# Optimization experiments

Measured on AMD Instinct MI355X. Metric: run time of the kernel, lower is better.

## Reference

```python
import jax, jax.numpy as jnp
import numpy as np

L, B, H, R = 128, 4, 768, 24
LN_EPS = 1e-5


def setup_inputs() -> dict:
    key = jax.random.key(0)
    ks = jax.random.split(key, 10)
    s = 1.0 / np.sqrt(H)
    return {
        "h_re": jax.random.normal(ks[0], (L, B, H), jnp.float32),
        "h_share": jax.random.normal(ks[1], (L, B, H), jnp.float32),
        "mask": jnp.ones((L, B), jnp.float32),
        # r: Linear(2H -> H)
        "r_w": jax.random.normal(ks[2], (H, 2 * H), jnp.float32) * s,
        "r_b": jnp.zeros((H,), jnp.float32),
        # hid2hid: Linear(3H -> H)
        "hid_w": jax.random.normal(ks[3], (H, 3 * H), jnp.float32) * s,
        "hid_b": jnp.zeros((H,), jnp.float32),
        # LayerNorm(H)
        "ln_g": jnp.ones((H,), jnp.float32),
        "ln_b": jnp.zeros((H,), jnp.float32),
        # hid2rel: Linear(H -> R)
        "rel_w": jax.random.normal(ks[4], (R, H), jnp.float32) * s,
        "rel_b": jnp.zeros((R,), jnp.float32),
    }


def reference(h_re, h_share, mask, r_w, r_b, hid_w, hid_b, ln_g, ln_b, rel_w, rel_b):
    # h_global = max_over_length( tanh( Linear([h_share; h_re]) ) )  -> [B, H]
    # Decompose concat-linear into two additive projections (same math).
    w_sh, w_re = r_w[:, :H], r_w[:, H:]
    g = jnp.tanh(jnp.einsum('lbh,kh->lbk', h_share, w_sh)
                 + jnp.einsum('lbh,kh->lbk', h_re, w_re) + r_b)
    g = jnp.max(g, axis=0)  # [B, H]

    # hid2hid(cat(r1, r2, g)) = h_re@W1^T (bcast over j) + h_re@W2^T (bcast over i) + g@W3^T + b
    w1, w2, w3 = hid_w[:, :H], hid_w[:, H:2 * H], hid_w[:, 2 * H:]
    p1 = jnp.einsum('lbh,kh->lbk', h_re, w1)        # [L, B, H] -> varies with i
    p2 = jnp.einsum('lbh,kh->lbk', h_re, w2)        # [L, B, H] -> varies with j
    pg = jnp.einsum('bh,kh->bk', g, w3) + hid_b     # [B, H]
    z = p1[:, None, :, :] + p2[None, :, :, :] + pg  # [L, L, B, H]

    # LayerNorm over last dim
    mu = jnp.mean(z, axis=-1, keepdims=True)
    var = jnp.mean(jnp.square(z - mu), axis=-1, keepdims=True)
    z = (z - mu) * jax.lax.rsqrt(var + LN_EPS) * ln_g + ln_b

    # ELU (dropout = identity in eval), then sigmoid(hid2rel)
    z = jax.nn.elu(z)
    re = jax.nn.sigmoid(jnp.einsum('ijbh,rh->ijbr', z, rel_w) + rel_b)  # [L, L, B, R]

    # pairwise mask: mask[i,b] * mask[j,b]
    m = mask[:, None, :] * mask[None, :, :]        # [L, L, B]
    return re * m[..., None]
```

## Files before the change

kernel.cpp:

```cpp
#include <hip/hip_runtime.h>
#include <hip/hip_bf16.h>
#include <math.h>

#define L 128
#define B 4
#define H 768
#define LN_EPS 1e-5f
#define XROWS 272

typedef __attribute__((ext_vector_type(8))) short short8;
typedef __attribute__((ext_vector_type(4))) float f32x4;

static __device__ __forceinline__ unsigned f2bfu(float f) {
    unsigned u = __float_as_uint(f);
    return (u + 0x7FFFu + ((u >> 16) & 1u)) >> 16;
}
static __device__ __forceinline__ uint2 pk4(float4 v) {
    uint2 o;
    o.x = f2bfu(v.x) | (f2bfu(v.y) << 16);
    o.y = f2bfu(v.z) | (f2bfu(v.w) << 16);
    return o;
}
static __device__ __forceinline__ unsigned short f2b(float f) {
    union { __hip_bfloat16 h; unsigned short u; } cv;
    cv.h = __float2bfloat16(f);
    return cv.u;
}
static __device__ __forceinline__ unsigned fkey(float x) {
    unsigned u = __float_as_uint(x);
    return (u >> 31) ? ~u : (u | 0x80000000u);
}

__global__ __launch_bounds__(256) void kConv(const float* __restrict__ h_re,
                                             const float* __restrict__ h_share,
                                             const float* __restrict__ r_w,
                                             const float* __restrict__ hid_w,
                                             const float* __restrict__ rel_w,
                                             unsigned short* __restrict__ apack,
                                             unsigned short* __restrict__ wpackA,
                                             unsigned short* __restrict__ wpackB,
                                             unsigned short* __restrict__ rwb16,
                                             unsigned int* __restrict__ gmax) {
    int t = blockIdx.x * 256 + threadIdx.x;
    if (t >= 397056) return;
    if (t < 98304) {
        int m = t / 192, oct = t % 192, k = oct * 8;
        const float* src = (k < 768) ? (h_share + (size_t)m * 768 + k)
                                     : (h_re + (size_t)m * 768 + k - 768);
        float4 x = *(const float4*)src, y = *(const float4*)(src + 4);
        int mt = m >> 4, lr = m & 15, ks = k >> 5, lq = (k >> 3) & 3;
        uint2* dst = (uint2*)(apack + (((size_t)mt * 48 + ks) * 64 + lq * 16 + lr) * 8);
        dst[0] = pk4(x); dst[1] = pk4(y);
    } else if (t < 245760) {
        int t2 = t - 98304;
        int n = t2 / 192, oct = t2 % 192, k = oct * 8;
        const float* src = r_w + (size_t)n * 1536 + k;
        float4 x = *(const float4*)src, y = *(const float4*)(src + 4);
        int nt = n >> 4, lr = n & 15, ks = k >> 5, lq = (k >> 3) & 3;
        uint2* dst = (uint2*)(wpackA + (((size_t)nt * 48 + ks) * 64 + lq * 16 + lr) * 8);
        dst[0] = pk4(x); dst[1] = pk4(y);
    } else if (t < 393216) {
        int t3 = t - 245760;
        int n = t3 / 96, oct = t3 % 96, k = oct * 8;
        int half = (n >= 768) ? 1 : 0;
        const float* src = hid_w + (size_t)(n - half * 768) * 2304 + half * 768 + k;
        float4 x = *(const float4*)src, y = *(const float4*)(src + 4);
        int nt = n >> 4, lr = n & 15, ks = k >> 5, lq = (k >> 3) & 3;
        uint2* dst = (uint2*)(wpackB + (((size_t)nt * 24 + ks) * 64 + lq * 16 + lr) * 8);
        dst[0] = pk4(x); dst[1] = pk4(y);
    } else if (t < 396288) {
        int t4 = t - 393216;
        int nt = t4 / 1536, ks = (t4 / 64) % 24, l = t4 & 63;
        int row = nt * 16 + (l & 15);
        int k = ks * 32 + (l >> 4) * 8;
        uint2 o0 = make_uint2(0u, 0u), o1 = o0;
        if (row < 24) {
            const float* src = rel_w + (size_t)row * 768 + k;
            o0 = pk4(*(const float4*)src);
            o1 = pk4(*(const float4*)(src + 4));
        }
        uint2* dst = (uint2*)(rwb16 + (size_t)t4 * 8);
        dst[0] = o0; dst[1] = o1;
    } else {
        int t6 = t - 396288;
        gmax[t6] = 0u;
        gmax[768 + t6] = 0u;
        gmax[1536 + t6] = 0u;
        gmax[2304 + t6] = 0u;
    }
}

template<int KSW>
static __device__ __forceinline__ void gemm_steps(const unsigned short* __restrict__ a0p,
                                                  const unsigned short* __restrict__ a1p,
                                                  const unsigned short* __restrict__ w0p,
                                                  const unsigned short* __restrict__ w1p,
                                                  f32x4 acc[2][2]) {
#pragma unroll
    for (int s = 0; s < KSW; s++) {
        short8 a0 = *(const short8*)(a0p + (size_t)s * 512);
        short8 a1 = *(const short8*)(a1p + (size_t)s * 512);
        short8 w0 = *(const short8*)(w0p + (size_t)s * 512);
        short8 w1 = *(const short8*)(w1p + (size_t)s * 512);
        acc[0][0] = __builtin_amdgcn_mfma_f32_16x16x32_bf16(a0, w0, acc[0][0], 0, 0, 0);
        acc[0][1] = __builtin_amdgcn_mfma_f32_16x16x32_bf16(a0, w1, acc[0][1], 0, 0, 0);
        acc[1][0] = __builtin_amdgcn_mfma_f32_16x16x32_bf16(a1, w0, acc[1][0], 0, 0, 0);
        acc[1][1] = __builtin_amdgcn_mfma_f32_16x16x32_bf16(a1, w1, acc[1][1], 0, 0, 0);
    }
}

__global__ __launch_bounds__(256) void kGemm(const unsigned short* __restrict__ apack,
                                             const unsigned short* __restrict__ wpackA,
                                             const unsigned short* __restrict__ wpackB,
                                             unsigned int* __restrict__ gmax,
                                             unsigned short* __restrict__ xb16,
                                             unsigned short* __restrict__ vpack) {
    __shared__ float red[4][4][64][4];
    int id = blockIdx.x;
    int tid = threadIdx.x, lane = tid & 63, wv = tid >> 6;
    int lq = lane >> 4, lr = lane & 15;
    bool isA = id < 384;
    f32x4 acc[2][2] = {{{0.f,0.f,0.f,0.f},{0.f,0.f,0.f,0.f}},
                       {{0.f,0.f,0.f,0.f},{0.f,0.f,0.f,0.f}}};
    int mt0, nt0;
    if (isA) {
        mt0 = (id / 24) * 2; nt0 = (id % 24) * 2;
        const unsigned short* a0p = apack + ((size_t)mt0 * 48 + wv * 12) * 512 + lane * 8;
        const unsigned short* w0p = wpackA + ((size_t)nt0 * 48 + wv * 12) * 512 + lane * 8;
        gemm_steps<12>(a0p, a0p + 48 * 512, w0p, w0p + 48 * 512, acc);
    } else {
        int id2 = id - 384;
        mt0 = (id2 / 48) * 2; nt0 = (id2 % 48) * 2;
        const unsigned short* a0p = apack + ((size_t)mt0 * 48 + 24 + wv * 6) * 512 + lane * 8;
        const unsigned short* w0p = wpackB + ((size_t)nt0 * 24 + wv * 6) * 512 + lane * 8;
        gemm_steps<6>(a0p, a0p + 48 * 512, w0p, w0p + 24 * 512, acc);
    }
#pragma unroll
    for (int mi = 0; mi < 2; mi++)
#pragma unroll
        for (int ni = 0; ni < 2; ni++)
            *(f32x4*)&red[wv][mi * 2 + ni][lane][0] = acc[mi][ni];
    __syncthreads();
    if (wv != 0) return;

    f32x4 s2[2][2];
#pragma unroll
    for (int mi = 0; mi < 2; mi++)
#pragma unroll
        for (int ni = 0; ni < 2; ni++) {
            f32x4 v = *(f32x4*)&red[0][mi * 2 + ni][lane][0];
#pragma unroll
            for (int w = 1; w < 4; w++) {
                f32x4 u = *(f32x4*)&red[w][mi * 2 + ni][lane][0];
                v[0] += u[0]; v[1] += u[1]; v[2] += u[2]; v[3] += u[3];
            }
            s2[mi][ni] = v;
        }

    if (isA) {
#pragma unroll
        for (int ni = 0; ni < 2; ni++)
#pragma unroll
            for (int q = 0; q < 4; q++) {
                float mx = fmaxf(s2[0][ni][q], s2[1][ni][q]);
                mx = fmaxf(mx, __shfl_xor(mx, 16, 64));
                mx = fmaxf(mx, __shfl_xor(mx, 32, 64));
                if (lq == 0) {
                    int n = (nt0 + ni) * 16 + lr;
                    atomicMax(&gmax[q * 768 + n], fkey(mx));
                }
            }
    } else {
#pragma unroll
        for (int mi = 0; mi < 2; mi++)
#pragma unroll
            for (int ni = 0; ni < 2; ni++)
#pragma unroll
                for (int q = 0; q < 4; q++) {
                    int m = (mt0 + mi) * 16 + lq * 4 + q;
                    int n = (nt0 + ni) * 16 + lr;
                    int b = m & 3, l = m >> 2;
                    unsigned short val = f2b(s2[mi][ni][q]);
                    if (n < 768) {
                        xb16[((size_t)b * XROWS + l) * 768 + n] = val;
                    } else {
                        int k = n - 768;
                        size_t dst = ((((size_t)(b * 8 + (l >> 4)) * 24) + (k >> 5)) * 64
                                      + ((k >> 3) & 3) * 16 + (l & 15)) * 8 + (k & 7);
                        vpack[dst] = val;
                    }
                }
    }
}

__global__ __launch_bounds__(256) void kPg(const unsigned int* __restrict__ gmax,
                                           const float* __restrict__ r_b,
                                           const float* __restrict__ hid_w,
                                           const float* __restrict__ hid_b,
                                           unsigned short* __restrict__ xb16) {
    __shared__ float sg[768];
    __shared__ float sp[4][64];
    int kt = blockIdx.x, b = blockIdx.y, tid = threadIdx.x;
    for (int v = tid; v < 768; v += 256) {
        unsigned key = gmax[b * 768 + v];
        unsigned bits = (key & 0x80000000u) ? (key & 0x7FFFFFFFu) : ~key;
        sg[v] = tanhf(__uint_as_float(bits) + r_b[v]);
    }
    __syncthreads();
    int kk = tid & 63, hc = tid >> 6;
    int k = kt * 64 + kk;
    const float4* w4 = (const float4*)hid_w;
    const float4* g4 = (const float4*)sg;
    float acc = 0.f;
    for (int h = hc * 48; h < hc * 48 + 48; h++) {
        float4 gv = g4[h];
        float4 wv = w4[(size_t)k * 576 + 384 + h];
        acc += gv.x * wv.x + gv.y * wv.y + gv.z * wv.z + gv.w * wv.w;
    }
    sp[hc][kk] = acc;
    __syncthreads();
    if (hc == 0) {
        float pgv = sp[0][kk] + sp[1][kk] + sp[2][kk] + sp[3][kk] + hid_b[k];
        xb16[((size_t)b * XROWS + 256) * 768 + k] = f2b(pgv);
    }
}

__global__ __launch_bounds__(64, 4) void kC(const unsigned short* __restrict__ xb16,
                                            const unsigned short* __restrict__ vpack,
                                            const float* __restrict__ ln_g,
                                            const float* __restrict__ ln_b,
                                            const unsigned short* __restrict__ rwb16,
                                            const float* __restrict__ rel_b,
                                            const float* __restrict__ mask,
                                            float* __restrict__ out) {
    int i = blockIdx.x, b = blockIdx.y, jg = blockIdx.z;
    int lane = threadIdx.x;
    int lr = lane & 15, lh = lane >> 4;

    const unsigned short* p1r = xb16 + ((size_t)b * XROWS + i) * 768;
    const unsigned short* pgr = xb16 + ((size_t)b * XROWS + 256) * 768;
    const unsigned short* vfr = vpack + (((size_t)(b * 8 + jg) * 24) * 64 + (size_t)lane) * 8;

    float s1 = 0.f, s2 = 0.f;
#pragma unroll 4
    for (int s = 0; s < 24; s++) {
        int k = s * 32 + lh * 8;
        uint4 vv = *(const uint4*)(vfr + (size_t)s * 512);
        uint4 uu = *(const uint4*)(p1r + k);
        uint4 pp = *(const uint4*)(pgr + k);
        const unsigned* vw = (const unsigned*)&vv;
        const unsigned* uw = (const unsigned*)&uu;
        const unsigned* pw = (const unsigned*)&pp;
#pragma unroll
        for (int h = 0; h < 4; h++) {
            float z0 = __uint_as_float(vw[h] << 16) + __uint_as_float(uw[h] << 16)
                     + __uint_as_float(pw[h] << 16);
            float z1 = __uint_as_float(vw[h] & 0xffff0000u) + __uint_as_float(uw[h] & 0xffff0000u)
                     + __uint_as_float(pw[h] & 0xffff0000u);
            s1 += z0 + z1;
            s2 = fmaf(z0, z0, fmaf(z1, z1, s2));
        }
    }
    s1 += __shfl_xor(s1, 16, 64); s1 += __shfl_xor(s1, 32, 64);
    s2 += __shfl_xor(s2, 16, 64); s2 += __shfl_xor(s2, 32, 64);
    float mu  = s1 * (1.f / 768.f);
    float rs  = rsqrtf(s2 * (1.f / 768.f) - mu * mu + LN_EPS);
    float nmr = -mu * rs;

    f32x4 acc0 = {0.f, 0.f, 0.f, 0.f}, acc1 = {0.f, 0.f, 0.f, 0.f};
#pragma unroll 2
    for (int s = 0; s < 24; s++) {
        int k = s * 32 + lh * 8;
        uint4 vv = *(const uint4*)(vfr + (size_t)s * 512);
        uint4 uu = *(const uint4*)(p1r + k);
        uint4 pp = *(const uint4*)(pgr + k);
        float4 g0 = *(const float4*)(ln_g + k), g1 = *(const float4*)(ln_g + k + 4);
        float4 b0 = *(const float4*)(ln_b + k), b1 = *(const float4*)(ln_b + k + 4);
        const unsigned* vw = (const unsigned*)&vv;
        const unsigned* uw = (const unsigned*)&uu;
        const unsigned* pw = (const unsigned*)&pp;
        float ge[8] = {g0.x, g0.y, g0.z, g0.w, g1.x, g1.y, g1.z, g1.w};
        float be[8] = {b0.x, b0.y, b0.z, b0.w, b1.x, b1.y, b1.z, b1.w};
        short8 a;
#pragma unroll
        for (int h = 0; h < 4; h++) {
            float z0 = __uint_as_float(vw[h] << 16) + __uint_as_float(uw[h] << 16)
                     + __uint_as_float(pw[h] << 16);
            float z1 = __uint_as_float(vw[h] & 0xffff0000u) + __uint_as_float(uw[h] & 0xffff0000u)
                     + __uint_as_float(pw[h] & 0xffff0000u);
            float t0 = fmaf(fmaf(z0, rs, nmr), ge[2 * h], be[2 * h]);
            float t1 = fmaf(fmaf(z1, rs, nmr), ge[2 * h + 1], be[2 * h + 1]);
            t0 = fmaxf(t0, __expf(fminf(t0, 0.f)) - 1.f);
            t1 = fmaxf(t1, __expf(fminf(t1, 0.f)) - 1.f);
            a[2 * h]     = (short)f2b(t0);
            a[2 * h + 1] = (short)f2b(t1);
        }
        short8 bf0 = *(const short8*)(rwb16 + ((size_t)s * 64 + lane) * 8);
        short8 bf1 = *(const short8*)(rwb16 + ((size_t)(24 + s) * 64 + lane) * 8);
        acc0 = __builtin_amdgcn_mfma_f32_16x16x32_bf16(a, bf0, acc0, 0, 0, 0);
        acc1 = __builtin_amdgcn_mfma_f32_16x16x32_bf16(a, bf1, acc1, 0, 0, 0);
    }

    float mi_ = mask[i * 4 + b];
#pragma unroll
    for (int q = 0; q < 4; q++) {
        int jglob = jg * 16 + lh * 4 + q;
        float mval = mi_ * mask[jglob * 4 + b];
        size_t ob = ((size_t)(i * 128 + jglob) * 4 + b) * 24;
        out[ob + lr] = mval / (1.f + __expf(-(acc0[q] + rel_b[lr])));
        if (lr < 8)
            out[ob + 16 + lr] = mval / (1.f + __expf(-(acc1[q] + rel_b[16 + lr])));
    }
}

extern "C" void kernel_launch(void* const* d_in, const int* in_sizes, int n_in,
                              void* d_out, int out_size, void* d_ws, size_t ws_size,
                              hipStream_t stream) {
    const float* h_re    = (const float*)d_in[0];
    const float* h_share = (const float*)d_in[1];
    const float* mask    = (const float*)d_in[2];
    const float* r_w     = (const float*)d_in[3];
    const float* r_b     = (const float*)d_in[4];
    const float* hid_w   = (const float*)d_in[5];
    const float* hid_b   = (const float*)d_in[6];
    const float* ln_g    = (const float*)d_in[7];
    const float* ln_b    = (const float*)d_in[8];
    const float* rel_w   = (const float*)d_in[9];
    const float* rel_b   = (const float*)d_in[10];
    float* out = (float*)d_out;

    float* ws = (float*)d_ws;
    unsigned short* apack  = (unsigned short*)(ws);
    unsigned short* wpackA = (unsigned short*)(ws + 393216);
    unsigned short* wpackB = (unsigned short*)(ws + 983040);
    unsigned short* xb16   = (unsigned short*)(ws + 1572864);
    unsigned short* vpack  = (unsigned short*)(ws + 1990656);
    unsigned int*   gmax   = (unsigned int*)(ws + 2187264);
    unsigned short* rwb16  = (unsigned short*)(ws + 2190336);

    kConv<<<1552, 256, 0, stream>>>(h_re, h_share, r_w, hid_w, rel_w,
                                    apack, wpackA, wpackB, rwb16, gmax);
    kGemm<<<1152, 256, 0, stream>>>(apack, wpackA, wpackB, gmax, xb16, vpack);
    kPg<<<dim3(12, 4), 256, 0, stream>>>(gmax, r_b, hid_w, hid_b, xb16);
    kC<<<dim3(128, 4, 8), 64, 0, stream>>>(xb16, vpack, ln_g, ln_b, rwb16,
                                           rel_b, mask, out);
}
```

Before: 70.53 us.

## Compute LayerNorm statistics algebraically from row sums and cross dot products

Removes the per-pair statistics pass in kC by expanding the mean and variance of z = p1_i + p2_j + pg. That expansion needs per-row sums and squared sums, the cross dot-product matrix p1·p2^T (an MFMA GEMM in a new kDotS kernel), and dot products with pg, which a new single-kernel-per-batch kPgX produces. kGemm also writes p1 in the packed MFMA layout so these GEMMs can read it. In exchange there is an extra launch, and the pg matvec now runs on only 4 blocks, which may serialize the hid_w reads. Computing variance as E[z²]-mu² also raises the risk of cancellation error.

```diff
diff --git a/kernel.cpp b/kernel.cpp
--- a/kernel.cpp
+++ b/kernel.cpp
@@ -25,6 +25,9 @@
     union { __hip_bfloat16 h; unsigned short u; } cv;
     cv.h = __float2bfloat16(f);
     return cv.u;
+}
+static __device__ __forceinline__ float b2f(unsigned short u) {
+    return __uint_as_float(((unsigned)u) << 16);
 }
 static __device__ __forceinline__ unsigned fkey(float x) {
     unsigned u = __float_as_uint(x);
@@ -114,7 +117,8 @@
                                              const unsigned short* __restrict__ wpackB,
                                              unsigned int* __restrict__ gmax,
                                              unsigned short* __restrict__ xb16,
-                                             unsigned short* __restrict__ vpack) {
+                                             unsigned short* __restrict__ vpack,
+                                             unsigned short* __restrict__ p1pack) {
     __shared__ float red[4][4][64][4];
     int id = blockIdx.x;
     int tid = threadIdx.x, lane = tid & 63, wv = tid >> 6;
@@ -183,6 +187,9 @@
                     unsigned short val = f2b(s2[mi][ni][q]);
                     if (n < 768) {
                         xb16[((size_t)b * XROWS + l) * 768 + n] = val;
+                        size_t dst = ((((size_t)(b * 8 + (l >> 4)) * 24) + (n >> 5)) * 64
+                                      + ((n >> 3) & 3) * 16 + (l & 15)) * 8 + (n & 7);
+                        p1pack[dst] = val;
                     } else {
                         int k = n - 768;
                         size_t dst = ((((size_t)(b * 8 + (l >> 4)) * 24) + (k >> 5)) * 64
@@ -193,35 +200,154 @@
     }
 }
 
-__global__ __launch_bounds__(256) void kPg(const unsigned int* __restrict__ gmax,
-                                           const float* __restrict__ r_b,
-                                           const float* __restrict__ hid_w,
-                                           const float* __restrict__ hid_b,
-                                           unsigned short* __restrict__ xb16) {
+__global__ __launch_bounds__(256) void kDotS(const unsigned short* __restrict__ p1pack,
+                                             const unsigned short* __restrict__ vpack,
+                                             float* __restrict__ Dp,
+                                             float* __restrict__ Sp1,
+                                             float* __restrict__ Sp1q,
+                                             float* __restrict__ Sv1,
+                                             float* __restrict__ Sv2) {
+    __shared__ float red[4][4][64][4];
+    int id = blockIdx.x;
+    int tid = threadIdx.x, lane = tid & 63, wv = tid >> 6;
+    int lq = lane >> 4, lr = lane & 15;
+    if (id < 64) {
+        int b = id >> 4, tile = id & 15, it = tile >> 2, jt = tile & 3;
+        f32x4 acc[2][2] = {{{0.f,0.f,0.f,0.f},{0.f,0.f,0.f,0.f}},
+                           {{0.f,0.f,0.f,0.f},{0.f,0.f,0.f,0.f}}};
+        const unsigned short* a0p = p1pack + (((size_t)(b * 8 + it * 2) * 24) + wv * 6) * 512 + lane * 8;
+        const unsigned short* a1p = p1pack + (((size_t)(b * 8 + it * 2 + 1) * 24) + wv * 6) * 512 + lane * 8;
+        const unsigned short* w0p = vpack + (((size_t)(b * 8 + jt * 2) * 24) + wv * 6) * 512 + lane * 8;
+        const unsigned short* w1p = vpack + (((size_t)(b * 8 + jt * 2 + 1) * 24) + wv * 6) * 512 + lane * 8;
+        gemm_steps<6>(a0p, a1p, w0p, w1p, acc);
+#pragma unroll
+        for (int mi = 0; mi < 2; mi++)
+#pragma unroll
+            for (int ni = 0; ni < 2; ni++)
+                *(f32x4*)&red[wv][mi * 2 + ni][lane][0] = acc[mi][ni];
+        __syncthreads();
+        if (wv != 0) return;
+#pragma unroll
+        for (int mi = 0; mi < 2; mi++)
+#pragma unroll
+            for (int ni = 0; ni < 2; ni++) {
+                f32x4 v = *(f32x4*)&red[0][mi * 2 + ni][lane][0];
+#pragma unroll
+                for (int w = 1; w < 4; w++) {
+                    f32x4 u = *(f32x4*)&red[w][mi * 2 + ni][lane][0];
+                    v[0] += u[0]; v[1] += u[1]; v[2] += u[2]; v[3] += u[3];
+                }
+#pragma unroll
+                for (int q = 0; q < 4; q++) {
+                    int i = it * 32 + mi * 16 + lq * 4 + q;
+                    int j = jt * 32 + ni * 16 + lr;
+                    Dp[((size_t)b * 128 + i) * 128 + j] = v[q];
+                }
+            }
+    } else {
+        int t = (id - 64) * 4 + wv;
+        bool isP = t < 32;
+        int t2 = t & 31;
+        int b = t2 >> 3, tile = t2 & 7;
+        const unsigned short* src = (isP ? p1pack : vpack)
+                                    + ((size_t)(b * 8 + tile) * 24) * 512 + lane * 8;
+        float s1 = 0.f, sq = 0.f;
+        for (int s = 0; s < 24; s++) {
+            uint4 x = *(const uint4*)(src + (size_t)s * 512);
+            const unsigned* xw = (const unsigned*)&x;
+#pragma unroll
+            for (int h = 0; h < 4; h++) {
+                float e0 = __uint_as_float(xw[h] << 16);
+                float e1 = __uint_as_float(xw[h] & 0xffff0000u);
+                s1 += e0 + e1;
+                sq = fmaf(e0, e0, fmaf(e1, e1, sq));
+            }
+        }
+        s1 += __shfl_xor(s1, 16, 64); s1 += __shfl_xor(s1, 32, 64);
+        sq += __shfl_xor(sq, 16, 64); sq += __shfl_xor(sq, 32, 64);
+        if (lq == 0) {
+            int row = tile * 16 + lr;
+            if (isP) { Sp1[b * 128 + row] = s1; Sp1q[b * 128 + row] = sq; }
+            else     { Sv1[b * 128 + row] = s1; Sv2[b * 128 + row] = sq; }
+        }
+    }
+}
+
+__global__ __launch_bounds__(256) void kPgX(const unsigned int* __restrict__ gmax,
+                                            const float* __restrict__ r_b,
+                                            const float* __restrict__ hid_w,
+                                            const float* __restrict__ hid_b,
+                                            const unsigned short* __restrict__ p1pack,
+                                            const unsigned short* __restrict__ vpack,
+                                            unsigned short* __restrict__ xb16,
+                                            float* __restrict__ Spg,
+                                            float* __restrict__ Spg2,
+                                            float* __restrict__ Cp1,
+                                            float* __restrict__ Cv) {
     __shared__ float sg[768];
-    __shared__ float sp[4][64];
-    int kt = blockIdx.x, b = blockIdx.y, tid = threadIdx.x;
+    __shared__ float spg[768];
+    __shared__ float rbuf[8];
+    int b = blockIdx.x, tid = threadIdx.x;
+    int lane = tid & 63, wv = tid >> 6, lq = lane >> 4, lr = lane & 15;
+
     for (int v = tid; v < 768; v += 256) {
         unsigned key = gmax[b * 768 + v];
         unsigned bits = (key & 0x80000000u) ? (key & 0x7FFFFFFFu) : ~key;
         sg[v] = tanhf(__uint_as_float(bits) + r_b[v]);
     }
     __syncthreads();
-    int kk = tid & 63, hc = tid >> 6;
-    int k = kt * 64 + kk;
     const float4* w4 = (const float4*)hid_w;
     const float4* g4 = (const float4*)sg;
-    float acc = 0.f;
-    for (int h = hc * 48; h < hc * 48 + 48; h++) {
-        float4 gv = g4[h];
-        float4 wv = w4[(size_t)k * 576 + 384 + h];
-        acc += gv.x * wv.x + gv.y * wv.y + gv.z * wv.z + gv.w * wv.w;
-    }
-    sp[hc][kk] = acc;
+#pragma unroll
+    for (int kk = 0; kk < 3; kk++) {
+        int k = tid + kk * 256;
+        float acc = 0.f;
+        for (int h = 0; h < 192; h++) {
+            float4 gv = g4[h];
+            float4 ww = w4[(size_t)k * 576 + 384 + h];
+            acc += gv.x * ww.x + gv.y * ww.y + gv.z * ww.z + gv.w * ww.w;
+        }
+        unsigned short pb = f2b(acc + hid_b[k]);
+        xb16[((size_t)b * XROWS + 256) * 768 + k] = pb;
+        spg[k] = b2f(pb);
+    }
     __syncthreads();
-    if (hc == 0) {
-        float pgv = sp[0][kk] + sp[1][kk] + sp[2][kk] + sp[3][kk] + hid_b[k];
-        xb16[((size_t)b * XROWS + 256) * 768 + k] = f2b(pgv);
+    float l1 = 0.f, l2 = 0.f;
+    for (int v = tid; v < 768; v += 256) { float x = spg[v]; l1 += x; l2 = fmaf(x, x, l2); }
+#pragma unroll
+    for (int off = 32; off > 0; off >>= 1) {
+        l1 += __shfl_xor(l1, off, 64);
+        l2 += __shfl_xor(l2, off, 64);
+    }
+    if (lane == 0) { rbuf[wv] = l1; rbuf[4 + wv] = l2; }
+    __syncthreads();
+    if (tid == 0) {
+        Spg[b]  = rbuf[0] + rbuf[1] + rbuf[2] + rbuf[3];
+        Spg2[b] = rbuf[4] + rbuf[5] + rbuf[6] + rbuf[7];
+    }
+    for (int gi = 0; gi < 4; gi++) {
+        int g = wv + gi * 4;
+        int side = g >> 3, tile = g & 7;
+        const unsigned short* src = (side ? vpack : p1pack)
+                                    + ((size_t)(b * 8 + tile) * 24) * 512 + lane * 8;
+        float d = 0.f;
+        for (int s = 0; s < 24; s++) {
+            uint4 x = *(const uint4*)(src + (size_t)s * 512);
+            const unsigned* xw = (const unsigned*)&x;
+            int kb = s * 32 + lq * 8;
+#pragma unroll
+            for (int h = 0; h < 4; h++) {
+                float e0 = __uint_as_float(xw[h] << 16);
+                float e1 = __uint_as_float(xw[h] & 0xffff0000u);
+                d = fmaf(e0, spg[kb + 2 * h], fmaf(e1, spg[kb + 2 * h + 1], d));
+            }
+        }
+        d += __shfl_xor(d, 16, 64); d += __shfl_xor(d, 32, 64);
+        if (lq == 0) {
+            int row = tile * 16 + lr;
+            if (side) Cv[b * 128 + row] = d;
+            else      Cp1[b * 128 + row] = d;
+        }
     }
 }
 
@@ -232,40 +358,32 @@
                                             const unsigned short* __restrict__ rwb16,
                                             const float* __restrict__ rel_b,
                                             const float* __restrict__ mask,
+                                            const float* __restrict__ Dp,
+                                            const float* __restrict__ Sp1,
+                                            const float* __restrict__ Sp1q,
+                                            const float* __restrict__ Sv1,
+                                            const float* __restrict__ Sv2,
+                                            const float* __restrict__ Spg,
+                                            const float* __restrict__ Spg2,
+                                            const float* __restrict__ Cp1,
+                                            const float* __restrict__ Cv,
                                             float* __restrict__ out) {
     int i = blockIdx.x, b = blockIdx.y, jg = blockIdx.z;
     int lane = threadIdx.x;
     int lr = lane & 15, lh = lane >> 4;
+    int j = jg * 16 + lr;
+
+    float s1 = Sp1[b * 128 + i] + Spg[b] + Sv1[b * 128 + j];
+    float s2 = Sp1q[b * 128 + i] + Spg2[b] + Sv2[b * 128 + j]
+             + 2.f * (Dp[((size_t)b * 128 + i) * 128 + j]
+                      + Cp1[b * 128 + i] + Cv[b * 128 + j]);
+    float mu  = s1 * (1.f / 768.f);
+    float rs  = rsqrtf(s2 * (1.f / 768.f) - mu * mu + LN_EPS);
+    float nmr = -mu * rs;
 
     const unsigned short* p1r = xb16 + ((size_t)b * XROWS + i) * 768;
     const unsigned short* pgr = xb16 + ((size_t)b * XROWS + 256) * 768;
     const unsigned short* vfr = vpack + (((size_t)(b * 8 + jg) * 24) * 64 + (size_t)lane) * 8;
-
-    float s1 = 0.f, s2 = 0.f;
-#pragma unroll 4
-    for (int s = 0; s < 24; s++) {
-        int k = s * 32 + lh * 8;
-        uint4 vv = *(const uint4*)(vfr + (size_t)s * 512);
-        uint4 uu = *(const uint4*)(p1r + k);
-        uint4 pp = *(const uint4*)(pgr + k);
-        const unsigned* vw = (const unsigned*)&vv;
-        const unsigned* uw = (const unsigned*)&uu;
-        const unsigned* pw = (const unsigned*)&pp;
-#pragma unroll
-        for (int h = 0; h < 4; h++) {
-            float z0 = __uint_as_float(vw[h] << 16) + __uint_as_float(uw[h] << 16)
-                     + __uint_as_float(pw[h] << 16);
-            float z1 = __uint_as_float(vw[h] & 0xffff0000u) + __uint_as_float(uw[h] & 0xffff0000u)
-                     + __uint_as_float(pw[h] & 0xffff0000u);
-            s1 += z0 + z1;
-            s2 = fmaf(z0, z0, fmaf(z1, z1, s2));
-        }
-    }
-    s1 += __shfl_xor(s1, 16, 64); s1 += __shfl_xor(s1, 32, 64);
-    s2 += __shfl_xor(s2, 16, 64); s2 += __shfl_xor(s2, 32, 64);
-    float mu  = s1 * (1.f / 768.f);
-    float rs  = rsqrtf(s2 * (1.f / 768.f) - mu * mu + LN_EPS);
-    float nmr = -mu * rs;
 
     f32x4 acc0 = {0.f, 0.f, 0.f, 0.f}, acc1 = {0.f, 0.f, 0.f, 0.f};
 #pragma unroll 2
@@ -335,13 +453,27 @@
     unsigned short* wpackB = (unsigned short*)(ws + 983040);
     unsigned short* xb16   = (unsigned short*)(ws + 1572864);
     unsigned short* vpack  = (unsigned short*)(ws + 1990656);
-    unsigned int*   gmax   = (unsigned int*)(ws + 2187264);
-    unsigned short* rwb16  = (unsigned short*)(ws + 2190336);
+    unsigned short* p1pack = (unsigned short*)(ws + 2187264);
+    float*          Dp     = ws + 2383872;
+    unsigned int*   gmax   = (unsigned int*)(ws + 2449408);
+    unsigned short* rwb16  = (unsigned short*)(ws + 2452480);
+    float*          Sp1    = ws + 2464768;
+    float*          Sp1q   = ws + 2465280;
+    float*          Sv1    = ws + 2465792;
+    float*          Sv2    = ws + 2466304;
+    float*          Cp1    = ws + 2466816;
+    float*          Cv     = ws + 2467328;
+    float*          SpgB   = ws + 2467840;
+    float*          Spg2B  = ws + 2467844;
 
     kConv<<<1552, 256, 0, stream>>>(h_re, h_share, r_w, hid_w, rel_w,
                                     apack, wpackA, wpackB, rwb16, gmax);
-    kGemm<<<1152, 256, 0, stream>>>(apack, wpackA, wpackB, gmax, xb16, vpack);
-    kPg<<<dim3(12, 4), 256, 0, stream>>>(gmax, r_b, hid_w, hid_b, xb16);
+    kGemm<<<1152, 256, 0, stream>>>(apack, wpackA, wpackB, gmax, xb16,
+                                    vpack, p1pack);
+    kDotS<<<80, 256, 0, stream>>>(p1pack, vpack, Dp, Sp1, Sp1q, Sv1, Sv2);
+    kPgX<<<4, 256, 0, stream>>>(gmax, r_b, hid_w, hid_b, p1pack, vpack,
+                                xb16, SpgB, Spg2B, Cp1, Cv);
     kC<<<dim3(128, 4, 8), 64, 0, stream>>>(xb16, vpack, ln_g, ln_b, rwb16,
-                                           rel_b, mask, out);
-}
+                                           rel_b, mask, Dp, Sp1, Sp1q,
+                                           Sv1, Sv2, SpgB, Spg2B, Cp1, Cv, out);
+}
```

After: 139.1 us. 1.97x slower.
